# Performance work log

Measured on AMD Instinct MI355X. Metric: run time of the kernel, lower is better.

## Reference

```python
import jax, jax.numpy as jnp
import numpy as np

NUM_STEPS = 8
SLOPE = 25.0        # snntorch surrogate.fast_sigmoid default slope
MAX_STD = 2.0
MIN_STD = 0.1
STATE_DIM = 6
HIDDEN = 128
OUT = 1
BATCH = 65536
W_STD = 0.01


@jax.custom_vjp
def spike(x):
    # heaviside(x) with fast-sigmoid surrogate gradient
    return (x > 0).astype(x.dtype)

def _spike_fwd(x):
    return spike(x), x

def _spike_bwd(x, g):
    return (g / (SLOPE * jnp.abs(x) + 1.0) ** 2,)

spike.defvjp(_spike_fwd, _spike_bwd)


def setup_inputs() -> dict:
    key = jax.random.key(0)
    ks = jax.random.split(key, 8)
    state = jax.random.normal(ks[0], (BATCH, STATE_DIM), dtype=jnp.float32)
    w_fc1 = W_STD * jax.random.normal(ks[1], (HIDDEN, STATE_DIM), dtype=jnp.float32)
    w_rec1 = W_STD * jax.random.normal(ks[2], (HIDDEN, HIDDEN), dtype=jnp.float32)
    w_fc2 = W_STD * jax.random.normal(ks[3], (HIDDEN, HIDDEN), dtype=jnp.float32)
    w_rec2 = W_STD * jax.random.normal(ks[4], (HIDDEN, HIDDEN), dtype=jnp.float32)
    w_mean = W_STD * jax.random.normal(ks[5], (OUT, HIDDEN), dtype=jnp.float32)
    w_std = W_STD * jax.random.normal(ks[6], (OUT, HIDDEN), dtype=jnp.float32)
    return {
        "state": state,
        "w_fc1": w_fc1, "w_rec1": w_rec1,
        "w_fc2": w_fc2, "w_rec2": w_rec2,
        "w_mean": w_mean, "w_std": w_std,
        "alpha1": jnp.float32(0.9), "beta1": jnp.float32(0.9), "thr1": jnp.float32(1.0),
        "alpha2": jnp.float32(0.9), "beta2": jnp.float32(0.9), "thr2": jnp.float32(1.0),
    }


def _snn_forward(state, w_fc1, w_rec1, w_fc2, w_rec2, w_mean, w_std,
                 alpha1, beta1, thr1, alpha2, beta2, thr2):
    a1 = jnp.clip(alpha1, 0.0, 1.0); b1 = jnp.clip(beta1, 0.0, 1.0)
    a2 = jnp.clip(alpha2, 0.0, 1.0); b2 = jnp.clip(beta2, 0.0, 1.0)

    B = state.shape[0]
    cur1_in = state @ w_fc1.T  # constant across steps: [B, H]
    z = jnp.zeros((B, HIDDEN), dtype=state.dtype)

    def step(carry, _):
        syn1, mem1, spk1, syn2, mem2, spk2 = carry
        # layer 1: snntorch Synaptic (reset-by-subtract, reset from prev mem, detached)
        reset1 = jax.lax.stop_gradient((mem1 - thr1 > 0).astype(mem1.dtype))
        syn1 = a1 * syn1 + cur1_in + spk1 @ w_rec1.T
        mem1 = b1 * mem1 + syn1 - reset1 * thr1
        spk1 = spike(mem1 - thr1)
        # layer 2
        reset2 = jax.lax.stop_gradient((mem2 - thr2 > 0).astype(mem2.dtype))
        syn2 = a2 * syn2 + spk1 @ w_fc2.T + spk2 @ w_rec2.T
        mem2 = b2 * mem2 + syn2 - reset2 * thr2
        spk2 = spike(mem2 - thr2)
        return (syn1, mem1, spk1, syn2, mem2, spk2), spk2

    init = (z, z, z, z, z, z)
    _, spk_rec = jax.lax.scan(step, init, None, length=NUM_STEPS)  # [T, B, H]
    avg_spikes = spk_rec.mean(axis=0)  # [B, H]

    value_mean = jnp.tanh(avg_spikes @ w_mean.T)
    value_std = (MAX_STD - MIN_STD) * jax.nn.sigmoid(avg_spikes @ w_std.T + 2.0) + MIN_STD
    return value_mean, value_std


def reference(state, w_fc1, w_rec1, w_fc2, w_rec2, w_mean, w_std,
              alpha1, beta1, thr1, alpha2, beta2, thr2):
    return _snn_forward(state, w_fc1, w_rec1, w_fc2, w_rec2, w_mean, w_std,
                        alpha1, beta1, thr1, alpha2, beta2, thr2)
```

## Files before the change

kernel.cpp:

```cpp
#include <hip/hip_runtime.h>
#include <cmath>


constexpr int BATCH = 65536;
constexpr int HID   = 128;
constexpr int SDIM  = 6;
constexpr int NSTEP = 8;
constexpr int BLOCK = 1024;
constexpr int GRID  = 256;
constexpr int WAVES_TOTAL = GRID * (BLOCK / 64);
constexpr int ELEMS_PER_WAVE = BATCH / WAVES_TOTAL;

__global__ __launch_bounds__(BLOCK) void snn_fwd(
    const float* __restrict__ state,
    const float* __restrict__ w_fc1,
    const float* __restrict__ w_rec1,
    const float* __restrict__ w_fc2,
    const float* __restrict__ w_rec2,
    const float* __restrict__ w_mean,
    const float* __restrict__ w_std,
    const float* __restrict__ p_alpha1, const float* __restrict__ p_beta1,
    const float* __restrict__ p_thr1,
    const float* __restrict__ p_alpha2, const float* __restrict__ p_beta2,
    const float* __restrict__ p_thr2,
    float* __restrict__ out)
{
    __shared__ float2 ld_rec1[HID * 64];
    __shared__ float2 ld_fc2 [HID * 64];
    __shared__ float2 ld_fc1 [SDIM * 64];
    __shared__ float  ld_wm[HID];
    __shared__ float  ld_wsd[HID];

    const int tid = threadIdx.x;

    for (int v = tid; v < HID * 64; v += BLOCK) {
        const int l = v >> 7;
        const int j = v & 127;
        const int pos = (j << 6) | (l ^ (j & 63));
        ld_rec1[pos] = make_float2(w_rec1[l * HID + j], w_rec1[(l + 64) * HID + j]);
        ld_fc2 [pos] = make_float2(w_fc2 [l * HID + j], w_fc2 [(l + 64) * HID + j]);
    }
    for (int v = tid; v < SDIM * 64; v += BLOCK) {
        const int k = v >> 6, l = v & 63;
        ld_fc1[(k << 6) | l] = make_float2(w_fc1[l * SDIM + k], w_fc1[(l + 64) * SDIM + k]);
    }
    if (tid < HID)               ld_wm [tid]        = w_mean[tid];
    else if (tid < 2 * HID)      ld_wsd[tid - HID]  = w_std [tid - HID];

    const float a1 = fminf(fmaxf(p_alpha1[0], 0.f), 1.f);
    const float b1 = fminf(fmaxf(p_beta1 [0], 0.f), 1.f);
    const float a2 = fminf(fmaxf(p_alpha2[0], 0.f), 1.f);
    const float b2 = fminf(fmaxf(p_beta2 [0], 0.f), 1.f);
    const float t1 = p_thr1[0];
    const float t2 = p_thr2[0];

    __syncthreads();

    const int lane  = tid & 63;
    const int gwave = blockIdx.x * (BLOCK / 64) + (tid >> 6);

    for (int e = 0; e < ELEMS_PER_WAVE; ++e) {
        const int b = gwave + WAVES_TOTAL * e;

        float cur_a = 0.f, cur_b = 0.f;
        #pragma unroll
        for (int k = 0; k < SDIM; ++k) {
            const float s = state[b * SDIM + k];
            const float2 w = ld_fc1[(k << 6) | lane];
            cur_a = fmaf(s, w.x, cur_a);
            cur_b = fmaf(s, w.y, cur_b);
        }

        float syn1a = 0.f, syn1b = 0.f, mem1a = 0.f, mem1b = 0.f;
        float syn2a = 0.f, syn2b = 0.f, mem2a = 0.f, mem2b = 0.f;
        bool  spk1a = false, spk1b = false, spk2a = false, spk2b = false;
        float cnt_a = 0.f, cnt_b = 0.f;
        unsigned long long m1a = 0ull, m1b = 0ull, m2a = 0ull, m2b = 0ull;

        #pragma unroll 1
        for (int t = 0; t < NSTEP; ++t) {
            float r_a = 0.f, r_b = 0.f;
            unsigned long long m = m1a;
            while (m) {
                const int j = __builtin_ctzll(m); m &= m - 1;
                const float2 w = ld_rec1[(j << 6) | (lane ^ j)];
                r_a += w.x; r_b += w.y;
            }
            m = m1b;
            while (m) {
                const int j0 = __builtin_ctzll(m); m &= m - 1;
                const int j = j0 + 64;
                const float2 w = ld_rec1[(j << 6) | (lane ^ j0)];
                r_a += w.x; r_b += w.y;
            }
            syn1a = fmaf(a1, syn1a, cur_a + r_a);
            syn1b = fmaf(a1, syn1b, cur_b + r_b);
            mem1a = fmaf(b1, mem1a, syn1a) - (spk1a ? t1 : 0.f);
            mem1b = fmaf(b1, mem1b, syn1b) - (spk1b ? t1 : 0.f);
            spk1a = (mem1a - t1) > 0.f;
            spk1b = (mem1b - t1) > 0.f;
            m1a = __ballot(spk1a);
            m1b = __ballot(spk1b);

            float f_a = 0.f, f_b = 0.f;
            m = m1a;
            while (m) {
                const int j = __builtin_ctzll(m); m &= m - 1;
                const float2 w = ld_fc2[(j << 6) | (lane ^ j)];
                f_a += w.x; f_b += w.y;
            }
            m = m1b;
            while (m) {
                const int j0 = __builtin_ctzll(m); m &= m - 1;
                const int j = j0 + 64;
                const float2 w = ld_fc2[(j << 6) | (lane ^ j0)];
                f_a += w.x; f_b += w.y;
            }
            m = m2a;
            while (m) {
                const int j = __builtin_ctzll(m); m &= m - 1;
                f_a += w_rec2[lane * HID + j];
                f_b += w_rec2[(lane + 64) * HID + j];
            }
            m = m2b;
            while (m) {
                const int j = __builtin_ctzll(m) + 64; m &= m - 1;
                f_a += w_rec2[lane * HID + j];
                f_b += w_rec2[(lane + 64) * HID + j];
            }
            syn2a = fmaf(a2, syn2a, f_a);
            syn2b = fmaf(a2, syn2b, f_b);
            mem2a = fmaf(b2, mem2a, syn2a) - (spk2a ? t2 : 0.f);
            mem2b = fmaf(b2, mem2b, syn2b) - (spk2b ? t2 : 0.f);
            spk2a = (mem2a - t2) > 0.f;
            spk2b = (mem2b - t2) > 0.f;
            m2a = __ballot(spk2a);
            m2b = __ballot(spk2b);
            cnt_a += spk2a ? 1.f : 0.f;
            cnt_b += spk2b ? 1.f : 0.f;
        }

        const float avg_a = cnt_a * (1.f / (float)NSTEP);
        const float avg_b = cnt_b * (1.f / (float)NSTEP);
        float dm = avg_a * ld_wm [lane] + avg_b * ld_wm [lane + 64];
        float ds = avg_a * ld_wsd[lane] + avg_b * ld_wsd[lane + 64];
        #pragma unroll
        for (int off = 32; off > 0; off >>= 1) {
            dm += __shfl_xor(dm, off, 64);
            ds += __shfl_xor(ds, off, 64);
        }
        if (lane == 0) {
            out[b]         = tanhf(dm);
            const float sg = 1.f / (1.f + expf(-(ds + 2.f)));
            out[BATCH + b] = 1.9f * sg + 0.1f;
        }
    }
}

extern "C" void kernel_launch(void* const* d_in, const int* in_sizes, int n_in,
                              void* d_out, int out_size, void* d_ws, size_t ws_size,
                              hipStream_t stream) {
    (void)in_sizes; (void)n_in; (void)d_ws; (void)ws_size; (void)out_size;
    snn_fwd<<<GRID, BLOCK, 0, stream>>>(
        (const float*)d_in[0],
        (const float*)d_in[1],
        (const float*)d_in[2],
        (const float*)d_in[3],
        (const float*)d_in[4],
        (const float*)d_in[5],
        (const float*)d_in[6],
        (const float*)d_in[7],
        (const float*)d_in[8],
        (const float*)d_in[9],
        (const float*)d_in[10],
        (const float*)d_in[11],
        (const float*)d_in[12],
        (float*)d_out);
}
```

Baseline: 130.0 us.

## Drop LDS weight staging and gather sparse spike weights from global memory

```diff
diff --git a/kernel.cpp b/kernel.cpp
--- a/kernel.cpp
+++ b/kernel.cpp
@@ -6,12 +6,12 @@
 constexpr int HID   = 128;
 constexpr int SDIM  = 6;
 constexpr int NSTEP = 8;
-constexpr int BLOCK = 1024;
-constexpr int GRID  = 256;
+constexpr int BLOCK = 256;
+constexpr int GRID  = 2048;
 constexpr int WAVES_TOTAL = GRID * (BLOCK / 64);
 constexpr int ELEMS_PER_WAVE = BATCH / WAVES_TOTAL;
 
-__global__ __launch_bounds__(BLOCK) void snn_fwd(
+__global__ __launch_bounds__(BLOCK, 8) void snn_fwd(
     const float* __restrict__ state,
     const float* __restrict__ w_fc1,
     const float* __restrict__ w_rec1,
@@ -25,27 +25,18 @@
     const float* __restrict__ p_thr2,
     float* __restrict__ out)
 {
-    __shared__ float2 ld_rec1[HID * 64];
-    __shared__ float2 ld_fc2 [HID * 64];
-    __shared__ float2 ld_fc1 [SDIM * 64];
-    __shared__ float  ld_wm[HID];
-    __shared__ float  ld_wsd[HID];
+    const int tid   = threadIdx.x;
+    const int lane  = tid & 63;
+    const int gwave = blockIdx.x * (BLOCK / 64) + (tid >> 6);
 
-    const int tid = threadIdx.x;
-
-    for (int v = tid; v < HID * 64; v += BLOCK) {
-        const int l = v >> 7;
-        const int j = v & 127;
-        const int pos = (j << 6) | (l ^ (j & 63));
-        ld_rec1[pos] = make_float2(w_rec1[l * HID + j], w_rec1[(l + 64) * HID + j]);
-        ld_fc2 [pos] = make_float2(w_fc2 [l * HID + j], w_fc2 [(l + 64) * HID + j]);
+    float w1a[SDIM], w1b[SDIM];
+    #pragma unroll
+    for (int k = 0; k < SDIM; ++k) {
+        w1a[k] = w_fc1[lane * SDIM + k];
+        w1b[k] = w_fc1[(lane + 64) * SDIM + k];
     }
-    for (int v = tid; v < SDIM * 64; v += BLOCK) {
-        const int k = v >> 6, l = v & 63;
-        ld_fc1[(k << 6) | l] = make_float2(w_fc1[l * SDIM + k], w_fc1[(l + 64) * SDIM + k]);
-    }
-    if (tid < HID)               ld_wm [tid]        = w_mean[tid];
-    else if (tid < 2 * HID)      ld_wsd[tid - HID]  = w_std [tid - HID];
+    const float wm_a = w_mean[lane], wm_b = w_mean[lane + 64];
+    const float ws_a = w_std [lane], ws_b = w_std [lane + 64];
 
     const float a1 = fminf(fmaxf(p_alpha1[0], 0.f), 1.f);
     const float b1 = fminf(fmaxf(p_beta1 [0], 0.f), 1.f);
@@ -54,10 +45,12 @@
     const float t1 = p_thr1[0];
     const float t2 = p_thr2[0];
 
-    __syncthreads();
-
-    const int lane  = tid & 63;
-    const int gwave = blockIdx.x * (BLOCK / 64) + (tid >> 6);
+    const float* __restrict__ rec1_a = w_rec1 + lane * HID;
+    const float* __restrict__ rec1_b = w_rec1 + (lane + 64) * HID;
+    const float* __restrict__ fc2_a  = w_fc2  + lane * HID;
+    const float* __restrict__ fc2_b  = w_fc2  + (lane + 64) * HID;
+    const float* __restrict__ rec2_a = w_rec2 + lane * HID;
+    const float* __restrict__ rec2_b = w_rec2 + (lane + 64) * HID;
 
     for (int e = 0; e < ELEMS_PER_WAVE; ++e) {
         const int b = gwave + WAVES_TOTAL * e;
@@ -66,9 +59,8 @@
         #pragma unroll
         for (int k = 0; k < SDIM; ++k) {
             const float s = state[b * SDIM + k];
-            const float2 w = ld_fc1[(k << 6) | lane];
-            cur_a = fmaf(s, w.x, cur_a);
-            cur_b = fmaf(s, w.y, cur_b);
+            cur_a = fmaf(s, w1a[k], cur_a);
+            cur_b = fmaf(s, w1b[k], cur_b);
         }
 
         float syn1a = 0.f, syn1b = 0.f, mem1a = 0.f, mem1b = 0.f;
@@ -83,15 +75,12 @@
             unsigned long long m = m1a;
             while (m) {
                 const int j = __builtin_ctzll(m); m &= m - 1;
-                const float2 w = ld_rec1[(j << 6) | (lane ^ j)];
-                r_a += w.x; r_b += w.y;
+                r_a += rec1_a[j]; r_b += rec1_b[j];
             }
             m = m1b;
             while (m) {
-                const int j0 = __builtin_ctzll(m); m &= m - 1;
-                const int j = j0 + 64;
-                const float2 w = ld_rec1[(j << 6) | (lane ^ j0)];
-                r_a += w.x; r_b += w.y;
+                const int j = __builtin_ctzll(m) + 64; m &= m - 1;
+                r_a += rec1_a[j]; r_b += rec1_b[j];
             }
             syn1a = fmaf(a1, syn1a, cur_a + r_a);
             syn1b = fmaf(a1, syn1b, cur_b + r_b);
@@ -106,27 +95,22 @@
             m = m1a;
             while (m) {
                 const int j = __builtin_ctzll(m); m &= m - 1;
-                const float2 w = ld_fc2[(j << 6) | (lane ^ j)];
-                f_a += w.x; f_b += w.y;
+                f_a += fc2_a[j]; f_b += fc2_b[j];
             }
             m = m1b;
             while (m) {
-                const int j0 = __builtin_ctzll(m); m &= m - 1;
-                const int j = j0 + 64;
-                const float2 w = ld_fc2[(j << 6) | (lane ^ j0)];
-                f_a += w.x; f_b += w.y;
+                const int j = __builtin_ctzll(m) + 64; m &= m - 1;
+                f_a += fc2_a[j]; f_b += fc2_b[j];
             }
             m = m2a;
             while (m) {
                 const int j = __builtin_ctzll(m); m &= m - 1;
-                f_a += w_rec2[lane * HID + j];
-                f_b += w_rec2[(lane + 64) * HID + j];
+                f_a += rec2_a[j]; f_b += rec2_b[j];
             }
             m = m2b;
             while (m) {
                 const int j = __builtin_ctzll(m) + 64; m &= m - 1;
-                f_a += w_rec2[lane * HID + j];
-                f_b += w_rec2[(lane + 64) * HID + j];
+                f_a += rec2_a[j]; f_b += rec2_b[j];
             }
             syn2a = fmaf(a2, syn2a, f_a);
             syn2b = fmaf(a2, syn2b, f_b);
@@ -142,8 +126,8 @@
 
         const float avg_a = cnt_a * (1.f / (float)NSTEP);
         const float avg_b = cnt_b * (1.f / (float)NSTEP);
-        float dm = avg_a * ld_wm [lane] + avg_b * ld_wm [lane + 64];
-        float ds = avg_a * ld_wsd[lane] + avg_b * ld_wsd[lane + 64];
+        float dm = avg_a * wm_a + avg_b * wm_b;
+        float ds = avg_a * ws_a + avg_b * ws_b;
         #pragma unroll
         for (int off = 32; off > 0; off >>= 1) {
             dm += __shfl_xor(dm, off, 64);
```

After: 319.9 us. 146% more time.
